# Kernel optimization log

Hardware: AMD Instinct MI355X
Metric: run time of the kernel (lower is better)

Reference implementation:

```python
import jax, jax.numpy as jnp
import numpy as np

B, T, C = 8, 2048, 512   # batch, seq_len, channels (= output_size for residual)
H, K, D = 4, 128, 128    # heads, key_size, per-head value size
KS, DIL = 4, 4           # conv kernel size, dilation = kernal_size**block_id
BAND = 3                 # matrix_band_part num_lower = num_upper = 3
NEG = -10000000.0


def setup_inputs() -> dict:
    key = jax.random.key(0)
    ks = jax.random.split(key, 12)
    s = 0.02
    f32 = jnp.float32
    x = jax.random.normal(ks[0], (B, T, C), f32)
    # per-head q/k/v dense params (stacked over head axis)
    Wq = jax.random.normal(ks[1], (H, C, K), f32) * s
    bq = jnp.zeros((H, K), f32)
    Wk = jax.random.normal(ks[2], (H, C, K), f32) * s
    bk = jnp.zeros((H, K), f32)
    Wv = jax.random.normal(ks[3], (H, C, D), f32) * s
    bv = jnp.zeros((H, D), f32)
    # output combiner Dense(output_size)
    Wo = jax.random.normal(ks[4], (H * D, C), f32) * s
    bo = jnp.zeros((C,), f32)
    # causal dilated Conv1D: kernel layout WIO = (kernel, in, out)
    Wc = jax.random.normal(ks[5], (KS, C, C), f32) * s
    bc = jnp.zeros((C,), f32)
    return {"x": x, "Wq": Wq, "bq": bq, "Wk": Wk, "bk": bk,
            "Wv": Wv, "bv": bv, "Wo": Wo, "bo": bo, "Wc": Wc, "bc": bc}


def reference(x, Wq, bq, Wk, bk, Wv, bv, Wo, bo, Wc, bc):
    # per-head projections: [B,H,T,K/D]
    q = jnp.einsum('btc,hck->bhtk', x, Wq) + bq[None, :, None, :]
    k = jnp.einsum('btc,hck->bhtk', x, Wk) + bk[None, :, None, :]
    v = jnp.einsum('btc,hcd->bhtd', x, Wv) + bv[None, :, None, :]
    # dense scores then band mask (faithful to matrix_band_part + abs>0 mask)
    sim = jnp.einsum('bhtk,bhsk->bhts', q, k) / jnp.sqrt(jnp.float32(K))
    idx = jnp.arange(T)
    band = (jnp.abs(idx[:, None] - idx[None, :]) <= BAND).astype(sim.dtype)
    simb = sim * band
    mask = jnp.where(jnp.abs(simb) > 0.0, 0.0, 1.0).astype(sim.dtype)
    att = jax.nn.softmax(simb + NEG * mask, axis=-1)
    heads = jnp.einsum('bhts,bhsd->bhtd', att, v)          # [B,H,T,D]
    cat = heads.transpose(0, 2, 1, 3).reshape(B, T, H * D)  # concat heads
    out = cat @ Wo + bo                                     # Dense(512)
    # causal dilated conv + relu
    pad = (KS - 1) * DIL
    conv = jax.lax.conv_general_dilated(
        out, Wc, window_strides=(1,), padding=[(pad, 0)],
        rhs_dilation=(DIL,), dimension_numbers=('NWC', 'WIO', 'NWC'))
    conv = jax.nn.relu(conv + bc)
    res = conv + x
    return jnp.where(res >= 0, res, 0.2 * res)  # leaky_relu(alpha=0.2)
```

## Files before the change

kernel.cpp:

```cpp
#include <hip/hip_runtime.h>
#include <math.h>

#define Bb    8
#define Tseq  2048
#define Cch   512
#define Mrows 16384
#define Nqkv  1536

typedef __bf16 bf16x8 __attribute__((ext_vector_type(8)));
typedef __bf16 bf16x4 __attribute__((ext_vector_type(4)));
typedef float  f32x4  __attribute__((ext_vector_type(4)));

__device__ __forceinline__ void gld_lds16(const void* g, void* l) {
  __builtin_amdgcn_global_load_lds(
      (const __attribute__((address_space(1))) unsigned int*)g,
      (__attribute__((address_space(3))) unsigned int*)l, 16, 0, 0);
}

__device__ __forceinline__ void swizzle_mn(int* m0, int* n0) {
  const int NX = gridDim.x;
  const int total = NX * gridDim.y;
  const int lid = blockIdx.y * NX + blockIdx.x;
  const int xcd = lid & 7;
  const int chunk = lid >> 3;
  const int idx = xcd * (total >> 3) + chunk;
  const int mt = idx / NX;
  const int nt = idx - mt * NX;
  *m0 = mt * 128;
  *n0 = nt * 128;
}

__global__ __launch_bounds__(256, 2) void gemm_bt_bf16_kernel(
    const __bf16* __restrict__ A, int lda,
    const __bf16* __restrict__ Bt, int K,
    const float* __restrict__ b0, const float* __restrict__ b1,
    const float* __restrict__ b2,
    __bf16* __restrict__ out, int ldo) {
  __shared__ __align__(16) __bf16 As[128 * 64];
  __shared__ __align__(16) __bf16 Bs[128 * 64];
  const int tid = threadIdx.x;
  const int w = tid >> 6, lane = tid & 63;
  const int wm = w & 1, wn = w >> 1;
  const int lm = lane & 15, quad = lane >> 4;
  int m0, n0;
  swizzle_mn(&m0, &n0);
  f32x4 acc[4][4] = {};
  for (int k0 = 0; k0 < K; k0 += 64) {
#pragma unroll
    for (int it = 0; it < 4; ++it) {
      const int c = w * 4 + it;
      const int e = c * 512 + lane * 8;
      const int row = e >> 6, col = e & 63;
      gld_lds16(A + (size_t)(m0 + row) * lda + k0 + col, &As[c * 512]);
      gld_lds16(Bt + (size_t)(n0 + row) * K + k0 + col, &Bs[c * 512]);
    }
    __syncthreads();
#pragma unroll
    for (int ks = 0; ks < 2; ++ks) {
      bf16x8 af[4], bfr[4];
#pragma unroll
      for (int i = 0; i < 4; ++i)
        af[i] = *(const bf16x8*)&As[(wm * 64 + i * 16 + lm) * 64 + ks * 32 + quad * 8];
#pragma unroll
      for (int j = 0; j < 4; ++j)
        bfr[j] = *(const bf16x8*)&Bs[(wn * 64 + j * 16 + lm) * 64 + ks * 32 + quad * 8];
#pragma unroll
      for (int i = 0; i < 4; ++i)
#pragma unroll
        for (int j = 0; j < 4; ++j)
          acc[i][j] = __builtin_amdgcn_mfma_f32_16x16x32_bf16(af[i], bfr[j], acc[i][j], 0, 0, 0);
    }
    __syncthreads();
  }
#pragma unroll
  for (int j = 0; j < 4; ++j) {
    const int col = n0 + wn * 64 + j * 16 + lm;
    const int s = col >> 9;
    const float* bp = (s == 0) ? b0 : (s == 1 ? b1 : b2);
    const float bias = bp[col & 511];
#pragma unroll
    for (int i = 0; i < 4; ++i) {
      const int row0 = m0 + wm * 64 + i * 16 + quad * 4;
#pragma unroll
      for (int r = 0; r < 4; ++r)
        out[(size_t)(row0 + r) * ldo + col] = (__bf16)(acc[i][j][r] + bias);
    }
  }
}

__global__ __launch_bounds__(256, 2) void gemm_wp_kernel(
    const __bf16* __restrict__ Wc_t, const __bf16* __restrict__ Wob,
    __bf16* __restrict__ Wp_bt) {
  __shared__ __align__(16) __bf16 As[128 * 64];
  __shared__ __align__(16) __bf16 Bs[128 * 64];
  const int tid = threadIdx.x;
  const int w = tid >> 6, lane = tid & 63;
  const int wm = w & 1, wn = w >> 1;
  const int lm = lane & 15, quad = lane >> 4;
  const int m0 = blockIdx.y * 128, n0 = blockIdx.x * 128;
  const __bf16* A = Wc_t + blockIdx.z * 512;
  __bf16* out = Wp_bt + blockIdx.z * 512;
  f32x4 acc[4][4] = {};
  for (int k0 = 0; k0 < 512; k0 += 64) {
#pragma unroll
    for (int it = 0; it < 4; ++it) {
      const int c = w * 4 + it;
      const int e = c * 512 + lane * 8;
      const int row = e >> 6, col = e & 63;
      gld_lds16(A + (size_t)(m0 + row) * 2048 + k0 + col, &As[c * 512]);
      gld_lds16(Wob + (size_t)(n0 + row) * 512 + k0 + col, &Bs[c * 512]);
    }
    __syncthreads();
#pragma unroll
    for (int ks = 0; ks < 2; ++ks) {
      bf16x8 af[4], bfr[4];
#pragma unroll
      for (int i = 0; i < 4; ++i)
        af[i] = *(const bf16x8*)&As[(wm * 64 + i * 16 + lm) * 64 + ks * 32 + quad * 8];
#pragma unroll
      for (int j = 0; j < 4; ++j)
        bfr[j] = *(const bf16x8*)&Bs[(wn * 64 + j * 16 + lm) * 64 + ks * 32 + quad * 8];
#pragma unroll
      for (int i = 0; i < 4; ++i)
#pragma unroll
        for (int j = 0; j < 4; ++j)
          acc[i][j] = __builtin_amdgcn_mfma_f32_16x16x32_bf16(af[i], bfr[j], acc[i][j], 0, 0, 0);
    }
    __syncthreads();
  }
#pragma unroll
  for (int j = 0; j < 4; ++j) {
    const int col = n0 + wn * 64 + j * 16 + lm;
#pragma unroll
    for (int i = 0; i < 4; ++i) {
      const int row0 = m0 + wm * 64 + i * 16 + quad * 4;
#pragma unroll
      for (int r = 0; r < 4; ++r)
        out[(size_t)(row0 + r) * 2048 + col] = (__bf16)(acc[i][j][r]);
    }
  }
}

__global__ __launch_bounds__(256, 2) void conv_gemm_kernel(
    const __bf16* __restrict__ A,
    const __bf16* __restrict__ Bt,
    const float* __restrict__ bc, const float* __restrict__ bj,
    const float* __restrict__ x, float* __restrict__ out,
    const __bf16* __restrict__ zeros) {
  __shared__ __align__(16) __bf16 As[128 * 64];
  __shared__ __align__(16) __bf16 Bs[128 * 64];
  const int tid = threadIdx.x;
  const int w = tid >> 6, lane = tid & 63;
  const int wm = w & 1, wn = w >> 1;
  const int lm = lane & 15, quad = lane >> 4;
  int m0, n0;
  swizzle_mn(&m0, &n0);
  f32x4 acc[4][4] = {};
  for (int k0 = 0; k0 < 4 * Cch; k0 += 64) {
    const int jtap = k0 >> 9;
    const int shift = 4 * jtap - 12;
    const int cin0 = k0 & 511;
#pragma unroll
    for (int it = 0; it < 4; ++it) {
      const int c = w * 4 + it;
      const int e = c * 512 + lane * 8;
      const int row = e >> 6, col = e & 63;
      const int m = m0 + row;
      const __bf16* src = (((m & (Tseq - 1)) + shift) >= 0)
                              ? A + (size_t)(m + shift) * Cch + cin0 + col
                              : zeros + (lane & 7) * 8;
      gld_lds16(src, &As[c * 512]);
      gld_lds16(Bt + (size_t)(n0 + row) * 2048 + k0 + col, &Bs[c * 512]);
    }
    __syncthreads();
#pragma unroll
    for (int ks = 0; ks < 2; ++ks) {
      bf16x8 af[4], bfr[4];
#pragma unroll
      for (int i = 0; i < 4; ++i)
        af[i] = *(const bf16x8*)&As[(wm * 64 + i * 16 + lm) * 64 + ks * 32 + quad * 8];
#pragma unroll
      for (int j = 0; j < 4; ++j)
        bfr[j] = *(const bf16x8*)&Bs[(wn * 64 + j * 16 + lm) * 64 + ks * 32 + quad * 8];
#pragma unroll
      for (int i = 0; i < 4; ++i)
#pragma unroll
        for (int j = 0; j < 4; ++j)
          acc[i][j] = __builtin_amdgcn_mfma_f32_16x16x32_bf16(af[i], bfr[j], acc[i][j], 0, 0, 0);
    }
    __syncthreads();
  }
#pragma unroll
  for (int j = 0; j < 4; ++j) {
    const int col = n0 + wn * 64 + j * 16 + lm;
    const float bcv = bc[col];
    float suf[4];
    suf[3] = bj[3 * 512 + col];
    suf[2] = suf[3] + bj[2 * 512 + col];
    suf[1] = suf[2] + bj[1 * 512 + col];
    suf[0] = suf[1] + bj[0 * 512 + col];
#pragma unroll
    for (int i = 0; i < 4; ++i) {
      const int row0 = m0 + wm * 64 + i * 16 + quad * 4;
#pragma unroll
      for (int r = 0; r < 4; ++r) {
        const int row = row0 + r;
        const int tl = row & (Tseq - 1);
        int jm = 15 - tl;
        jm = (jm < 0) ? 0 : (jm >> 2);
        float v = acc[i][j][r] + bcv + suf[jm];
        v = fmaxf(v, 0.f);
        v += x[(size_t)row * Cch + col];
        out[(size_t)row * Cch + col] = (v >= 0.f) ? v : 0.2f * v;
      }
    }
  }
}

__global__ __launch_bounds__(256) void attn_band_kernel(
    const __bf16* __restrict__ qkv, __bf16* __restrict__ cat) {
  const int tid = threadIdx.x;
  const int tsub = tid >> 4, g = tid & 15;
  const int t = blockIdx.x * 16 + tsub;
  const int bh = blockIdx.y;
  const int b = bh >> 2, h = bh & 3;
  const int d0 = g * 8;
  const size_t base = ((size_t)(b * Tseq + t)) * Nqkv + h * 128 + d0;
  bf16x8 qv = *(const bf16x8*)(qkv + base);
  const float scale = 0.08838834764831845f;
  float score[7];
#pragma unroll
  for (int i = 0; i < 7; ++i) {
    const int s = t - 3 + i;
    const bool valid = (s >= 0) && (s < Tseq);
    float p = 0.f;
    if (valid) {
      bf16x8 kv = *(const bf16x8*)(qkv + base + (size_t)(i - 3) * Nqkv + 512);
#pragma unroll
      for (int e = 0; e < 8; ++e) p += (float)qv[e] * (float)kv[e];
    }
    p += __shfl_xor(p, 1);
    p += __shfl_xor(p, 2);
    p += __shfl_xor(p, 4);
    p += __shfl_xor(p, 8);
    score[i] = valid ? p * scale : -1e30f;
  }
  float mx = score[0];
#pragma unroll
  for (int i = 1; i < 7; ++i) mx = fmaxf(mx, score[i]);
  float wgt[7], denom = 0.f;
#pragma unroll
  for (int i = 0; i < 7; ++i) {
    wgt[i] = (score[i] > -1e29f) ? expf(score[i] - mx) : 0.f;
    denom += wgt[i];
  }
  const float inv = 1.f / denom;
  float o[8] = {};
#pragma unroll
  for (int i = 0; i < 7; ++i) {
    if (wgt[i] != 0.f) {
      bf16x8 vv = *(const bf16x8*)(qkv + base + (size_t)(i - 3) * Nqkv + 1024);
#pragma unroll
      for (int e = 0; e < 8; ++e) o[e] += wgt[i] * (float)vv[e];
    }
  }
  bf16x8 ov;
#pragma unroll
  for (int e = 0; e < 8; ++e) ov[e] = (__bf16)(o[e] * inv);
  *(bf16x8*)(cat + ((size_t)(b * Tseq + t)) * Cch + h * 128 + d0) = ov;
}

#define PREP_A 8192
#define PREP_B 8960
#define PREP_C 9984
#define PREP_D 10240
#define PREP_E 10241
#define PREP_N 10273

__global__ __launch_bounds__(256) void prep_kernel(
    const float* __restrict__ x, const float* __restrict__ Wq,
    const float* __restrict__ Wk, const float* __restrict__ Wv,
    const float* __restrict__ Wo, const float* __restrict__ Wc,
    const float* __restrict__ bo,
    __bf16* __restrict__ xb, __bf16* __restrict__ Wqkv_t,
    __bf16* __restrict__ Wc_t, __bf16* __restrict__ Wob,
    float* __restrict__ bj, __bf16* __restrict__ zeros) {
  __shared__ float sArr[32][33];
  __shared__ float red[256];
  const int bid = blockIdx.x;
  const int tid = threadIdx.x;
  if (bid < PREP_A) {
    const size_t i = ((size_t)bid * 256 + tid) * 4;
    float4 v = *(const float4*)(x + i);
    bf16x4 o;
    o[0] = (__bf16)v.x; o[1] = (__bf16)v.y; o[2] = (__bf16)v.z; o[3] = (__bf16)v.w;
    *(bf16x4*)(xb + i) = o;
  } else if (bid < PREP_B) {
    const int l = bid - PREP_A;
    const int bx = l & 3, by = (l >> 2) & 15, z = l >> 6;
    const int sgrp = z >> 2, h = z & 3;
    const float* src = ((sgrp == 0) ? Wq : (sgrp == 1) ? Wk : Wv) + h * (512 * 128);
    __bf16* dst = Wqkv_t + (size_t)z * 128 * 512;
    const int tx = tid & 31, ty = tid >> 5;
    const int c0 = bx * 32, r0 = by * 32;
#pragma unroll
    for (int rr = 0; rr < 4; ++rr)
      sArr[ty + rr * 8][tx] = src[(size_t)(r0 + ty + rr * 8) * 128 + c0 + tx];
    __syncthreads();
#pragma unroll
    for (int rr = 0; rr < 4; ++rr)
      dst[(size_t)(c0 + ty + rr * 8) * 512 + r0 + tx] = (__bf16)sArr[tx][ty + rr * 8];
  } else if (bid < PREP_C) {
    const int l = bid - PREP_B;
    const int bx = l & 15, by = l >> 4;
    const int tx = tid & 31, ty = tid >> 5;
    const int c0 = bx * 32, r0 = by * 32;
#pragma unroll
    for (int rr = 0; rr < 4; ++rr)
      sArr[ty + rr * 8][tx] = Wc[(size_t)(r0 + ty + rr * 8) * 512 + c0 + tx];
    __syncthreads();
#pragma unroll
    for (int rr = 0; rr < 4; ++rr)
      Wc_t[(size_t)(c0 + ty + rr * 8) * 2048 + r0 + tx] = (__bf16)sArr[tx][ty + rr * 8];
  } else if (bid < PREP_D) {
    const int l = bid - PREP_C;
    const size_t i = ((size_t)l * 256 + tid) * 4;
    float4 v = *(const float4*)(Wo + i);
    bf16x4 o;
    o[0] = (__bf16)v.x; o[1] = (__bf16)v.y; o[2] = (__bf16)v.z; o[3] = (__bf16)v.w;
    *(bf16x4*)(Wob + i) = o;
  } else if (bid < PREP_E) {
    bf16x8 zero = {};
    *(bf16x8*)(zeros + tid * 8) = zero;
  } else {
    const int l = bid - PREP_E;
    const int j = l >> 3, nb = l & 7;
    const int n = nb * 64 + (tid & 63);
    const int cig = tid >> 6;
    const float* base = Wc + ((size_t)j * 512 + cig * 128) * 512 + n;
    float acc = 0.f;
#pragma unroll 8
    for (int ci = 0; ci < 128; ++ci) acc += bo[cig * 128 + ci] * base[(size_t)ci * 512];
    red[tid] = acc;
    __syncthreads();
    if (tid < 64)
      bj[j * 512 + n] = red[tid] + red[tid + 64] + red[tid + 128] + red[tid + 192];
  }
}

extern "C" void kernel_launch(void* const* d_in, const int* in_sizes, int n_in,
                              void* d_out, int out_size, void* d_ws, size_t ws_size,
                              hipStream_t stream) {
  const float* x  = (const float*)d_in[0];
  const float* Wq = (const float*)d_in[1];
  const float* bq = (const float*)d_in[2];
  const float* Wk = (const float*)d_in[3];
  const float* bk = (const float*)d_in[4];
  const float* Wv = (const float*)d_in[5];
  const float* bv = (const float*)d_in[6];
  const float* Wo = (const float*)d_in[7];
  const float* bo = (const float*)d_in[8];
  const float* Wc = (const float*)d_in[9];
  const float* bc = (const float*)d_in[10];
  float* out = (float*)d_out;

  char* p = (char*)d_ws;
  __bf16* xb     = (__bf16*)p;  p += (size_t)Mrows * Cch * 2;
  __bf16* qkv    = (__bf16*)p;  p += (size_t)Mrows * Nqkv * 2;
  __bf16* catb   = (__bf16*)p;  p += (size_t)Mrows * Cch * 2;
  __bf16* Wqkv_t = (__bf16*)p;  p += (size_t)Nqkv * Cch * 2;
  __bf16* Wc_t   = (__bf16*)p;  p += (size_t)Cch * 2048 * 2;
  __bf16* Wob    = (__bf16*)p;  p += (size_t)Cch * Cch * 2;
  __bf16* Wp_bt  = (__bf16*)p;  p += (size_t)Cch * 2048 * 2;
  float*  bj     = (float*)p;   p += 4 * Cch * 4;
  __bf16* zeros  = (__bf16*)p;  p += 4096;

  prep_kernel<<<PREP_N, 256, 0, stream>>>(x, Wq, Wk, Wv, Wo, Wc, bo,
                                          xb, Wqkv_t, Wc_t, Wob, bj, zeros);

  gemm_wp_kernel<<<dim3(4, 4, 4), 256, 0, stream>>>(Wc_t, Wob, Wp_bt);

  gemm_bt_bf16_kernel<<<dim3(Nqkv / 128, Mrows / 128), 256, 0, stream>>>(
      xb, Cch, Wqkv_t, Cch, bq, bk, bv, qkv, Nqkv);

  attn_band_kernel<<<dim3(Tseq / 16, Bb * 4), 256, 0, stream>>>(qkv, catb);

  conv_gemm_kernel<<<dim3(Cch / 128, Mrows / 128), 256, 0, stream>>>(
      catb, Wp_bt, bc, bj, x, out, zeros);
}
```

Baseline: 232.7 us.

## Swizzle LDS tile layout and merge QKV and weight-product GEMMs into one launch

Adds an XOR swizzle to the LDS tile layout of both GEMM kernels. Each 16-byte chunk's column group is XORed with row&7, which removes bank conflicts when fragments are read for MFMA. The QKV projection GEMM and the small Wc·Wo weight-product GEMM are also merged into a single launch of 1600 blocks, with work chosen by block index. This saves one kernel launch and lets the small GEMM fill otherwise idle slots, at the cost of extra branching and a bias path that is skipped for the weight-product blocks.

```diff
diff --git a/kernel.cpp b/kernel.cpp
--- a/kernel.cpp
+++ b/kernel.cpp
@@ -16,6 +16,8 @@
       (const __attribute__((address_space(1))) unsigned int*)g,
       (__attribute__((address_space(3))) unsigned int*)l, 16, 0, 0);
 }
+
+#define SWZ(r, g) (((r) << 6) + ((((g) ^ ((r) & 7))) << 3))
 
 __device__ __forceinline__ void swizzle_mn(int* m0, int* n0) {
   const int NX = gridDim.x;
@@ -30,65 +32,10 @@
   *n0 = nt * 128;
 }
 
-__global__ __launch_bounds__(256, 2) void gemm_bt_bf16_kernel(
-    const __bf16* __restrict__ A, int lda,
-    const __bf16* __restrict__ Bt, int K,
-    const float* __restrict__ b0, const float* __restrict__ b1,
-    const float* __restrict__ b2,
-    __bf16* __restrict__ out, int ldo) {
-  __shared__ __align__(16) __bf16 As[128 * 64];
-  __shared__ __align__(16) __bf16 Bs[128 * 64];
-  const int tid = threadIdx.x;
-  const int w = tid >> 6, lane = tid & 63;
-  const int wm = w & 1, wn = w >> 1;
-  const int lm = lane & 15, quad = lane >> 4;
-  int m0, n0;
-  swizzle_mn(&m0, &n0);
-  f32x4 acc[4][4] = {};
-  for (int k0 = 0; k0 < K; k0 += 64) {
-#pragma unroll
-    for (int it = 0; it < 4; ++it) {
-      const int c = w * 4 + it;
-      const int e = c * 512 + lane * 8;
-      const int row = e >> 6, col = e & 63;
-      gld_lds16(A + (size_t)(m0 + row) * lda + k0 + col, &As[c * 512]);
-      gld_lds16(Bt + (size_t)(n0 + row) * K + k0 + col, &Bs[c * 512]);
-    }
-    __syncthreads();
-#pragma unroll
-    for (int ks = 0; ks < 2; ++ks) {
-      bf16x8 af[4], bfr[4];
-#pragma unroll
-      for (int i = 0; i < 4; ++i)
-        af[i] = *(const bf16x8*)&As[(wm * 64 + i * 16 + lm) * 64 + ks * 32 + quad * 8];
-#pragma unroll
-      for (int j = 0; j < 4; ++j)
-        bfr[j] = *(const bf16x8*)&Bs[(wn * 64 + j * 16 + lm) * 64 + ks * 32 + quad * 8];
-#pragma unroll
-      for (int i = 0; i < 4; ++i)
-#pragma unroll
-        for (int j = 0; j < 4; ++j)
-          acc[i][j] = __builtin_amdgcn_mfma_f32_16x16x32_bf16(af[i], bfr[j], acc[i][j], 0, 0, 0);
-    }
-    __syncthreads();
-  }
-#pragma unroll
-  for (int j = 0; j < 4; ++j) {
-    const int col = n0 + wn * 64 + j * 16 + lm;
-    const int s = col >> 9;
-    const float* bp = (s == 0) ? b0 : (s == 1 ? b1 : b2);
-    const float bias = bp[col & 511];
-#pragma unroll
-    for (int i = 0; i < 4; ++i) {
-      const int row0 = m0 + wm * 64 + i * 16 + quad * 4;
-#pragma unroll
-      for (int r = 0; r < 4; ++r)
-        out[(size_t)(row0 + r) * ldo + col] = (__bf16)(acc[i][j][r] + bias);
-    }
-  }
-}
-
-__global__ __launch_bounds__(256, 2) void gemm_wp_kernel(
+__global__ __launch_bounds__(256, 2) void gemm_qkv_wp_kernel(
+    const __bf16* __restrict__ xb, const __bf16* __restrict__ Wqkv_t,
+    const float* __restrict__ bq, const float* __restrict__ bk,
+    const float* __restrict__ bv, __bf16* __restrict__ qkv,
     const __bf16* __restrict__ Wc_t, const __bf16* __restrict__ Wob,
     __bf16* __restrict__ Wp_bt) {
   __shared__ __align__(16) __bf16 As[128 * 64];
@@ -97,18 +44,37 @@
   const int w = tid >> 6, lane = tid & 63;
   const int wm = w & 1, wn = w >> 1;
   const int lm = lane & 15, quad = lane >> 4;
-  const int m0 = blockIdx.y * 128, n0 = blockIdx.x * 128;
-  const __bf16* A = Wc_t + blockIdx.z * 512;
-  __bf16* out = Wp_bt + blockIdx.z * 512;
+  const int srow = lane >> 3;
+  const int scol = (((lane & 7) ^ srow) << 3);
+  const int lid = blockIdx.x;
+
+  const __bf16 *Ap, *Bp;
+  __bf16* op;
+  int lda, ldo, m0, n0;
+  bool dobias;
+  if (lid < 1536) {
+    const int xcd = lid & 7, chunk = lid >> 3;
+    const int idx = xcd * 192 + chunk;
+    const int mt = idx / 12, nt = idx - mt * 12;
+    m0 = mt * 128; n0 = nt * 128;
+    Ap = xb; lda = 512; Bp = Wqkv_t;
+    op = qkv; ldo = 1536; dobias = true;
+  } else {
+    const int l2 = lid - 1536;
+    const int z = l2 >> 4;
+    m0 = ((l2 >> 2) & 3) * 128; n0 = (l2 & 3) * 128;
+    Ap = Wc_t + z * 512; lda = 2048; Bp = Wob;
+    op = Wp_bt + z * 512; ldo = 2048; dobias = false;
+  }
+
   f32x4 acc[4][4] = {};
   for (int k0 = 0; k0 < 512; k0 += 64) {
 #pragma unroll
     for (int it = 0; it < 4; ++it) {
       const int c = w * 4 + it;
-      const int e = c * 512 + lane * 8;
-      const int row = e >> 6, col = e & 63;
-      gld_lds16(A + (size_t)(m0 + row) * 2048 + k0 + col, &As[c * 512]);
-      gld_lds16(Wob + (size_t)(n0 + row) * 512 + k0 + col, &Bs[c * 512]);
+      const int row = c * 8 + srow;
+      gld_lds16(Ap + (size_t)(m0 + row) * lda + k0 + scol, &As[c * 512]);
+      gld_lds16(Bp + (size_t)(n0 + row) * 512 + k0 + scol, &Bs[c * 512]);
     }
     __syncthreads();
 #pragma unroll
@@ -116,10 +82,10 @@
       bf16x8 af[4], bfr[4];
 #pragma unroll
       for (int i = 0; i < 4; ++i)
-        af[i] = *(const bf16x8*)&As[(wm * 64 + i * 16 + lm) * 64 + ks * 32 + quad * 8];
+        af[i] = *(const bf16x8*)&As[SWZ(wm * 64 + i * 16 + lm, ks * 4 + quad)];
 #pragma unroll
       for (int j = 0; j < 4; ++j)
-        bfr[j] = *(const bf16x8*)&Bs[(wn * 64 + j * 16 + lm) * 64 + ks * 32 + quad * 8];
+        bfr[j] = *(const bf16x8*)&Bs[SWZ(wn * 64 + j * 16 + lm, ks * 4 + quad)];
 #pragma unroll
       for (int i = 0; i < 4; ++i)
 #pragma unroll
@@ -131,12 +97,18 @@
 #pragma unroll
   for (int j = 0; j < 4; ++j) {
     const int col = n0 + wn * 64 + j * 16 + lm;
+    float bias = 0.f;
+    if (dobias) {
+      const int s = col >> 9;
+      const float* bp = (s == 0) ? bq : (s == 1 ? bk : bv);
+      bias = bp[col & 511];
+    }
 #pragma unroll
     for (int i = 0; i < 4; ++i) {
       const int row0 = m0 + wm * 64 + i * 16 + quad * 4;
 #pragma unroll
       for (int r = 0; r < 4; ++r)
-        out[(size_t)(row0 + r) * 2048 + col] = (__bf16)(acc[i][j][r]);
+        op[(size_t)(row0 + r) * ldo + col] = (__bf16)(acc[i][j][r] + bias);
     }
   }
 }
@@ -153,6 +125,8 @@
   const int w = tid >> 6, lane = tid & 63;
   const int wm = w & 1, wn = w >> 1;
   const int lm = lane & 15, quad = lane >> 4;
+  const int srow = lane >> 3;
+  const int scol = (((lane & 7) ^ srow) << 3);
   int m0, n0;
   swizzle_mn(&m0, &n0);
   f32x4 acc[4][4] = {};
@@ -163,14 +137,13 @@
 #pragma unroll
     for (int it = 0; it < 4; ++it) {
       const int c = w * 4 + it;
-      const int e = c * 512 + lane * 8;
-      const int row = e >> 6, col = e & 63;
+      const int row = c * 8 + srow;
       const int m = m0 + row;
       const __bf16* src = (((m & (Tseq - 1)) + shift) >= 0)
-                              ? A + (size_t)(m + shift) * Cch + cin0 + col
-                              : zeros + (lane & 7) * 8;
+                              ? A + (size_t)(m + shift) * Cch + cin0 + scol
+                              : zeros + scol;
       gld_lds16(src, &As[c * 512]);
-      gld_lds16(Bt + (size_t)(n0 + row) * 2048 + k0 + col, &Bs[c * 512]);
+      gld_lds16(Bt + (size_t)(n0 + row) * 2048 + k0 + scol, &Bs[c * 512]);
     }
     __syncthreads();
 #pragma unroll
@@ -178,10 +151,10 @@
       bf16x8 af[4], bfr[4];
 #pragma unroll
       for (int i = 0; i < 4; ++i)
-        af[i] = *(const bf16x8*)&As[(wm * 64 + i * 16 + lm) * 64 + ks * 32 + quad * 8];
+        af[i] = *(const bf16x8*)&As[SWZ(wm * 64 + i * 16 + lm, ks * 4 + quad)];
 #pragma unroll
       for (int j = 0; j < 4; ++j)
-        bfr[j] = *(const bf16x8*)&Bs[(wn * 64 + j * 16 + lm) * 64 + ks * 32 + quad * 8];
+        bfr[j] = *(const bf16x8*)&Bs[SWZ(wn * 64 + j * 16 + lm, ks * 4 + quad)];
 #pragma unroll
       for (int i = 0; i < 4; ++i)
 #pragma unroll
@@ -378,10 +351,8 @@
   prep_kernel<<<PREP_N, 256, 0, stream>>>(x, Wq, Wk, Wv, Wo, Wc, bo,
                                           xb, Wqkv_t, Wc_t, Wob, bj, zeros);
 
-  gemm_wp_kernel<<<dim3(4, 4, 4), 256, 0, stream>>>(Wc_t, Wob, Wp_bt);
-
-  gemm_bt_bf16_kernel<<<dim3(Nqkv / 128, Mrows / 128), 256, 0, stream>>>(
-      xb, Cch, Wqkv_t, Cch, bq, bk, bv, qkv, Nqkv);
+  gemm_qkv_wp_kernel<<<1600, 256, 0, stream>>>(xb, Wqkv_t, bq, bk, bv, qkv,
+                                               Wc_t, Wob, Wp_bt);
 
   attn_band_kernel<<<dim3(Tseq / 16, Bb * 4), 256, 0, stream>>>(qkv, catb);
 
```

Result: faster. 214.6 us (-7.8%).
